# Optimization experiments

Measured on AMD Instinct MI355X. Metric: run time of the kernel, lower is better.

## Reference

```python
import jax, jax.numpy as jnp
import numpy as np

D = 4  # search range -> 2*D+1 = 9 correlation channels


def setup_inputs() -> dict:
    key = jax.random.key(0)
    k1, k2 = jax.random.split(key)
    N, C, H, W = 4, 128, 192, 640
    feature1 = jax.random.normal(k1, (N, C, H, W), dtype=jnp.float32)
    feature2 = jax.random.normal(k2, (N, C, H, W), dtype=jnp.float32)
    return {"feature1": feature1, "feature2": feature2}


def reference(feature1, feature2):
    # feature1, feature2: [N, C, H, W]
    N, C, H, W = feature1.shape
    d = D
    # Pad feature2 along width: [N, C, H, W + 2d]
    f2p = jnp.pad(feature2, ((0, 0), (0, 0), (0, 0), (d, d)))
    # For each shift i in [0, 2d], correlate feature1 with f2p[..., i:i+W]
    # and take the channel mean -> [N, 1, H, W]; concatenate over shifts.
    costs = [
        jnp.mean(feature1 * jax.lax.dynamic_slice_in_dim(f2p, i, W, axis=3),
                 axis=1, keepdims=True)
        for i in range(2 * d + 1)
    ]
    return jnp.concatenate(costs, axis=1)  # [N, 2d+1, H, W]
```

## Files before the change

### kernel.cpp

```cpp
#include <hip/hip_runtime.h>


constexpr int DD = 4;
constexpr int NS = 2 * DD + 1;
constexpr int N_ = 4, C_ = 128, H_ = 192, W_ = 640;
constexpr int HW = H_ * W_;
constexpr int SEGS  = W_ / 128;
constexpr int TILES = N_ * H_ * SEGS;
constexpr int WPB   = 4;
constexpr int NBLK  = TILES / WPB;

__global__ __launch_bounds__(256)
void cost_volume_kernel(const float* __restrict__ f1,
                        const float* __restrict__ f2,
                        float* __restrict__ out)
{
    const int lane = threadIdx.x & 63;
    const int wid  = blockIdx.x * WPB + (threadIdx.x >> 6);
    const int seg  = wid % SEGS;
    const int row  = wid / SEGS;
    const int n    = row / H_;
    const int h    = row - n * H_;
    const int w0   = seg * 128 + lane * 2;

    const size_t base = (size_t)n * C_ * HW + (size_t)h * W_;
    const float* f1p = f1 + base + w0;
    const float* f2p = f2 + base;

    float2 A[2];
    float2 B[2][5];

    auto load_stage = [&](int st, int c) {
        const float* f1c = f1p + (size_t)c * HW;
        const float* f2c = f2p + (size_t)c * HW;
        A[st] = *(const float2*)f1c;
#pragma unroll
        for (int k = 0; k < 5; ++k) {
            const int off = w0 - 4 + 2 * k;
            float2 v = make_float2(0.f, 0.f);
            if ((unsigned)off <= (unsigned)(W_ - 2))
                v = *(const float2*)(f2c + off);
            B[st][k] = v;
        }
    };

    float acc0[NS], acc1[NS];
#pragma unroll
    for (int i = 0; i < NS; ++i) { acc0[i] = 0.f; acc1[i] = 0.f; }

    load_stage(0, 0);
    load_stage(1, 1);

#pragma unroll 2
    for (int c = 0; c < C_; ++c) {
        const int st = c & 1;
        const float2 a = A[st];
        float v[10];
#pragma unroll
        for (int k = 0; k < 5; ++k) { v[2*k] = B[st][k].x; v[2*k+1] = B[st][k].y; }

#pragma unroll
        for (int i = 0; i < NS; ++i) {
            acc0[i] = fmaf(a.x, v[i],     acc0[i]);
            acc1[i] = fmaf(a.y, v[i + 1], acc1[i]);
        }

        if (c + 2 < C_) load_stage(st, c + 2);
    }

    constexpr float scale = 1.0f / (float)C_;
    float* orow = out + (size_t)n * NS * HW + (size_t)h * W_ + w0;
#pragma unroll
    for (int i = 0; i < NS; ++i) {
        float2 o;
        o.x = acc0[i] * scale;
        o.y = acc1[i] * scale;
        *(float2*)(orow + (size_t)i * HW) = o;
    }
}

extern "C" void kernel_launch(void* const* d_in, const int* in_sizes, int n_in,
                              void* d_out, int out_size, void* d_ws, size_t ws_size,
                              hipStream_t stream) {
    const float* f1 = (const float*)d_in[0];
    const float* f2 = (const float*)d_in[1];
    float* out = (float*)d_out;
    cost_volume_kernel<<<dim3(NBLK), dim3(256), 0, stream>>>(f1, f2, out);
}
```

Baseline: 518.0 us.

## Split channel reduction across two waves per tile with LDS combine and deeper prefetch

Each 128-pixel tile now gets a two-wave block. Each wave sums half of the channels, and the partial sums are combined through shared memory before the store. The prefetch depth goes from 2 to 4 stages, and the boundary branches on the f2 loads become clamped offsets with multiplicative masks. The aim is more memory-level parallelism and shorter per-wave serial chains in a bandwidth-bound kernel. The cost is extra registers, an LDS round trip, a block barrier and extra mask multiplies.

```diff
diff --git a/kernel.cpp b/kernel.cpp
--- a/kernel.cpp
+++ b/kernel.cpp
@@ -7,75 +7,94 @@
 constexpr int HW = H_ * W_;
 constexpr int SEGS  = W_ / 128;
 constexpr int TILES = N_ * H_ * SEGS;
-constexpr int WPB   = 4;
-constexpr int NBLK  = TILES / WPB;
+constexpr int CH    = C_ / 2;
+constexpr int PF    = 4;
 
-__global__ __launch_bounds__(256)
+__global__ __launch_bounds__(128, 6)
 void cost_volume_kernel(const float* __restrict__ f1,
                         const float* __restrict__ f2,
                         float* __restrict__ out)
 {
     const int lane = threadIdx.x & 63;
-    const int wid  = blockIdx.x * WPB + (threadIdx.x >> 6);
-    const int seg  = wid % SEGS;
-    const int row  = wid / SEGS;
+    const int half = threadIdx.x >> 6;
+    const int tile = blockIdx.x;
+    const int seg  = tile % SEGS;
+    const int row  = tile / SEGS;
     const int n    = row / H_;
     const int h    = row - n * H_;
     const int w0   = seg * 128 + lane * 2;
 
     const size_t base = (size_t)n * C_ * HW + (size_t)h * W_;
-    const float* f1p = f1 + base + w0;
-    const float* f2p = f2 + base;
+    const int    c0   = half * CH;
 
-    float2 A[2];
-    float2 B[2][5];
+    const float* f2b = f2 + base + (size_t)c0 * HW;
+    const float* f1p = f1 + base + (size_t)c0 * HW + w0;
 
-    auto load_stage = [&](int st, int c) {
-        const float* f1c = f1p + (size_t)c * HW;
-        const float* f2c = f2p + (size_t)c * HW;
-        A[st] = *(const float2*)f1c;
+    int   voff[5];
+    float mk[5];
 #pragma unroll
-        for (int k = 0; k < 5; ++k) {
-            const int off = w0 - 4 + 2 * k;
-            float2 v = make_float2(0.f, 0.f);
-            if ((unsigned)off <= (unsigned)(W_ - 2))
-                v = *(const float2*)(f2c + off);
-            B[st][k] = v;
-        }
+    for (int k = 0; k < 5; ++k) {
+        const int off   = w0 - 4 + 2 * k;
+        const bool ok   = (off >= 0) && (off <= W_ - 2);
+        voff[k] = ok ? off : 0;
+        mk[k]   = ok ? 1.f : 0.f;
+    }
+
+    float2 A[PF];
+    float2 B[PF][5];
+
+    auto load_stage = [&](int s, int c) {
+        A[s] = *(const float2*)(f1p + (size_t)c * HW);
+        const float* f2c = f2b + (size_t)c * HW;
+#pragma unroll
+        for (int k = 0; k < 5; ++k)
+            B[s][k] = *(const float2*)(f2c + voff[k]);
     };
 
     float acc0[NS], acc1[NS];
 #pragma unroll
     for (int i = 0; i < NS; ++i) { acc0[i] = 0.f; acc1[i] = 0.f; }
 
-    load_stage(0, 0);
-    load_stage(1, 1);
+#pragma unroll
+    for (int s = 0; s < PF; ++s) load_stage(s, s);
 
-#pragma unroll 2
-    for (int c = 0; c < C_; ++c) {
-        const int st = c & 1;
-        const float2 a = A[st];
+#pragma unroll 4
+    for (int c = 0; c < CH; ++c) {
+        const int s = c & (PF - 1);
+        const float2 a = A[s];
         float v[10];
 #pragma unroll
-        for (int k = 0; k < 5; ++k) { v[2*k] = B[st][k].x; v[2*k+1] = B[st][k].y; }
-
+        for (int k = 0; k < 5; ++k) {
+            v[2 * k]     = B[s][k].x * mk[k];
+            v[2 * k + 1] = B[s][k].y * mk[k];
+        }
 #pragma unroll
         for (int i = 0; i < NS; ++i) {
             acc0[i] = fmaf(a.x, v[i],     acc0[i]);
             acc1[i] = fmaf(a.y, v[i + 1], acc1[i]);
         }
-
-        if (c + 2 < C_) load_stage(st, c + 2);
+        if (c + PF < CH) load_stage(s, c + PF);
     }
 
-    constexpr float scale = 1.0f / (float)C_;
-    float* orow = out + (size_t)n * NS * HW + (size_t)h * W_ + w0;
+    __shared__ float red[NS][128];
+    if (half == 1) {
 #pragma unroll
-    for (int i = 0; i < NS; ++i) {
-        float2 o;
-        o.x = acc0[i] * scale;
-        o.y = acc1[i] * scale;
-        *(float2*)(orow + (size_t)i * HW) = o;
+        for (int i = 0; i < NS; ++i) {
+            red[i][2 * lane]     = acc0[i];
+            red[i][2 * lane + 1] = acc1[i];
+        }
+    }
+    __syncthreads();
+    if (half == 0) {
+        constexpr float scale = 1.0f / (float)C_;
+        float* orow = out + (size_t)n * NS * HW + (size_t)h * W_ + w0;
+#pragma unroll
+        for (int i = 0; i < NS; ++i) {
+            float2 o;
+            o.x = (acc0[i] + red[i][2 * lane])     * scale;
+            o.y = (acc1[i] + red[i][2 * lane + 1]) * scale;
+            *(float2*)(orow + (size_t)i * HW) = o;
+        }
     }
 }
 
@@ -85,5 +104,5 @@
     const float* f1 = (const float*)d_in[0];
     const float* f2 = (const float*)d_in[1];
     float* out = (float*)d_out;
-    cost_volume_kernel<<<dim3(NBLK), dim3(256), 0, stream>>>(f1, f2, out);
+    cost_volume_kernel<<<dim3(TILES), dim3(128), 0, stream>>>(f1, f2, out);
 }
```

New measurement: 1.393 ms. 169% more time.
